# Kernel optimization log

Hardware: AMD Instinct MI355X
Metric: run time of the kernel (lower is better)

Reference implementation:

```python
import jax, jax.numpy as jnp
import numpy as np

NUM_HEADS = 8

def setup_inputs() -> dict:
    key = jax.random.key(0)
    k1, k2, k3, k4 = jax.random.split(key, 4)
    B, N, S, C = 16, 256, 4096, 512
    return {
        "query": jax.random.normal(k1, (B, N, C), dtype=jnp.float32),
        "key": jax.random.normal(k2, (B, S, C), dtype=jnp.float32),
        "Wq": jax.random.normal(k3, (C, C), dtype=jnp.float32) * (C ** -0.5),
        "Wk": jax.random.normal(k4, (C, C), dtype=jnp.float32) * (C ** -0.5),
    }

def reference(query, key, Wq, Wk):
    B, N, C = query.shape
    S = key.shape[1]
    H = NUM_HEADS
    hd = C // H
    scale = hd ** -0.5
    # value = key (v_proj is Identity, value defaults to key)
    q = (query @ Wq).reshape(B, N, H, hd)   # b n h c
    k = (key @ Wk).reshape(B, S, H, hd)     # b s h c
    raw_attn = jnp.einsum('bnhc,bshc->bhns', q, k) * scale  # [B,H,N,S]
    # softmax over the QUERY axis (dim=-2), non-standard
    attn = jax.nn.softmax(raw_attn, axis=-2)
    # clamp-normalize over token axis; divisor is detached in the original
    div = jnp.clip(jnp.sum(attn, axis=-1, keepdims=True), 1.0, None)
    attn = attn / jax.lax.stop_gradient(div)
    # attn_drop has p=0.0 -> identity
    v = key.reshape(B, S, H, hd)
    out = jnp.einsum('bhns,bshc->bnhc', attn, v).reshape(B, N, C)
    # out_style = attn @ key_heads; since value == key this equals out
    out_style = out
    return out, out_style
```

## Files before the change

### kernel.cpp

```cpp
#include <hip/hip_runtime.h>
#include <hip/hip_bf16.h>


typedef __attribute__((ext_vector_type(8))) short bf16x8;
typedef __attribute__((ext_vector_type(4))) float f32x4;
typedef unsigned int u32;

__device__ __forceinline__ unsigned short f2bf(float f) {
  union { __hip_bfloat16 h; unsigned short u; } cv;
  cv.h = __float2bfloat16(f);
  return cv.u;
}

__device__ __forceinline__ u32 pkbf(float a, float b) {
  union { __hip_bfloat162 h; u32 u; } cv;
  cv.h = __float22bfloat162_rn(float2{a, b});
  return cv.u;
}

__device__ __forceinline__ void async_copy16(const void* gptr, void* lptr) {
  __builtin_amdgcn_global_load_lds((const __attribute__((address_space(1))) u32*)gptr,
                                   (__attribute__((address_space(3))) u32*)lptr,
                                   16, 0, 0);
}

__global__ __launch_bounds__(256) void prep_w(const float* __restrict__ Wq,
                                              const float* __restrict__ Wk,
                                              unsigned short* __restrict__ WtQ,
                                              unsigned short* __restrict__ WtK) {
  __shared__ float tile[64][65];
  const int blk = blockIdx.x;
  const float* W = (blk & 1) ? Wk : Wq;
  unsigned short* Wt = (blk & 1) ? WtK : WtQ;
  const int tb = blk >> 1;
  const int k0 = (tb >> 3) * 64, n0 = (tb & 7) * 64;
  const int t = threadIdx.x;
  const int row = t >> 4, col4 = (t & 15) * 4;
#pragma unroll
  for (int i = 0; i < 4; ++i) {
    int r = i * 16 + row;
    float4 v = *reinterpret_cast<const float4*>(&W[(size_t)(k0 + r) * 512 + n0 + col4]);
    tile[r][col4 + 0] = v.x; tile[r][col4 + 1] = v.y;
    tile[r][col4 + 2] = v.z; tile[r][col4 + 3] = v.w;
  }
  __syncthreads();
#pragma unroll
  for (int i = 0; i < 4; ++i) {
    int r = i * 16 + row;
    short4 s;
    s.x = (short)f2bf(tile[col4 + 0][r]);
    s.y = (short)f2bf(tile[col4 + 1][r]);
    s.z = (short)f2bf(tile[col4 + 2][r]);
    s.w = (short)f2bf(tile[col4 + 3][r]);
    *reinterpret_cast<short4*>(&Wt[(size_t)(n0 + r) * 512 + k0 + col4]) = s;
  }
}

__global__ __launch_bounds__(256, 3) void gemm_xw(const float* __restrict__ X,
                                                  const unsigned short* __restrict__ Wt,
                                                  __hip_bfloat16* __restrict__ Y) {
  __shared__ float As[128 * 64];
  __shared__ unsigned short Bs[128 * 64];
  const int t = threadIdx.x;
  const int wave = t >> 6, lane = t & 63, l15 = lane & 15, quad = lane >> 4;
  const int n0 = blockIdx.x * 128, m0 = blockIdx.y * 128;
  const int wm = (wave >> 1) * 64, wn = (wave & 1) * 64;

  const int a_rl = lane >> 4;
  const int b_rl = lane >> 3;
  const int b_cs = (lane & 7) ^ b_rl;

  f32x4 acc[4][4];
#pragma unroll
  for (int i = 0; i < 4; ++i)
#pragma unroll
    for (int j = 0; j < 4; ++j) { f32x4 z = {0.f, 0.f, 0.f, 0.f}; acc[i][j] = z; }

  for (int k0 = 0; k0 < 512; k0 += 64) {
    __syncthreads();
    {
      const float* aBase = X + (size_t)m0 * 512 + k0;
#pragma unroll
      for (int o = 0; o < 8; ++o) {
        int rg = wave * 8 + o;
        int r = rg * 4 + a_rl;
        int cs = (lane & 15) ^ (r & 7);
        async_copy16(aBase + (size_t)r * 512 + cs * 4, &As[rg * 256]);
      }
      const unsigned short* bBase = Wt + (size_t)n0 * 512 + k0;
#pragma unroll
      for (int o = 0; o < 4; ++o) {
        int rg = wave * 4 + o;
        int r = rg * 8 + b_rl;
        async_copy16(bBase + (size_t)r * 512 + b_cs * 8, &Bs[rg * 512]);
      }
    }
    __syncthreads();

#pragma unroll
    for (int x = 0; x < 2; ++x) {
      bf16x8 a[4], bfr[4];
#pragma unroll
      for (int i = 0; i < 4; ++i) {
        int ra = wm + 16 * i + l15;
        int c0 = x * 8 + quad * 2;
        float4 f0 = *reinterpret_cast<const float4*>(&As[(ra * 16 + (c0 ^ (ra & 7))) * 4]);
        float4 f1 = *reinterpret_cast<const float4*>(&As[(ra * 16 + ((c0 + 1) ^ (ra & 7))) * 4]);
        union { bf16x8 v; unsigned short s[8]; } u;
        u.s[0] = f2bf(f0.x); u.s[1] = f2bf(f0.y); u.s[2] = f2bf(f0.z); u.s[3] = f2bf(f0.w);
        u.s[4] = f2bf(f1.x); u.s[5] = f2bf(f1.y); u.s[6] = f2bf(f1.z); u.s[7] = f2bf(f1.w);
        a[i] = u.v;
      }
#pragma unroll
      for (int j = 0; j < 4; ++j) {
        int rb = wn + 16 * j + l15;
        int cb = x * 4 + quad;
        bfr[j] = *reinterpret_cast<const bf16x8*>(&Bs[(rb * 8 + (cb ^ (rb & 7))) * 8]);
      }
#pragma unroll
      for (int i = 0; i < 4; ++i)
#pragma unroll
        for (int j = 0; j < 4; ++j)
          acc[i][j] = __builtin_amdgcn_mfma_f32_16x16x32_bf16(a[i], bfr[j], acc[i][j], 0, 0, 0);
    }
  }
#pragma unroll
  for (int i = 0; i < 4; ++i)
#pragma unroll
    for (int j = 0; j < 4; ++j)
#pragma unroll
      for (int r = 0; r < 4; ++r) {
        int m = m0 + wm + 16 * i + 4 * quad + r;
        int n = n0 + wn + 16 * j + l15;
        Y[(size_t)m * 512 + n] = __float2bfloat16(acc[i][j][r]);
      }
}

__global__ __launch_bounds__(512, 2) void attn_kernel(const __hip_bfloat16* __restrict__ qg,
                                                      const __hip_bfloat16* __restrict__ kg,
                                                      const float* __restrict__ keyg,
                                                      float* __restrict__ accg,
                                                      float* __restrict__ rsg) {
  __shared__ unsigned short qs[256 * 64];
  __shared__ unsigned short vs[64 * 128];
  __shared__ unsigned short pst[256 * 128];

  const int t = threadIdx.x;
  const int wave = t >> 6, lane = t & 63, l15 = lane & 15, quad = lane >> 4;
  const int blk = blockIdx.x, chunk = blk & 1, bh = blk >> 1, b = bh >> 3, h = bh & 7;
  const int l7 = l15 & 7;

  {
    const unsigned short* qbase = (const unsigned short*)qg + (size_t)(b * 256) * 512 + h * 64;
#pragma unroll
    for (int i = 0; i < 4; ++i) {
      int lin = i * 512 + t;
      int n = lin >> 3, cc = lin & 7, phys = cc ^ (n & 7);
      bf16x8 v = *reinterpret_cast<const bf16x8*>(qbase + (size_t)n * 512 + cc * 8);
      *reinterpret_cast<bf16x8*>(&qs[n * 64 + phys * 8]) = v;
    }
  }

  const unsigned short* kbase = (const unsigned short*)kg + (size_t)(b * 4096 + chunk * 2048) * 512 + h * 64;
  const float* vbase = keyg + (size_t)(b * 4096 + chunk * 2048) * 512 + h * 64;

  bf16x8 kc0 = *reinterpret_cast<const bf16x8*>(kbase + (size_t)(16 * wave + l15) * 512 + quad * 8);
  bf16x8 kc1 = *reinterpret_cast<const bf16x8*>(kbase + (size_t)(16 * wave + l15) * 512 + 32 + quad * 8);
  float vbuf[16];
#pragma unroll
  for (int half = 0; half < 2; ++half) {
    int sc = wave + 8 * half;
#pragma unroll
    for (int j = 0; j < 8; ++j)
      vbuf[half * 8 + j] = vbase[(size_t)(sc * 8 + j) * 512 + lane];
  }

  union { bf16x8 f; int w[4]; } ones_u;
  ones_u.w[0] = 0x3F803F80; ones_u.w[1] = 0x3F803F80;
  ones_u.w[2] = 0x3F803F80; ones_u.w[3] = 0x3F803F80;
  const bf16x8 ones = ones_u.f;

  f32x4 oacc[2][4], rsacc[2];
#pragma unroll
  for (int i = 0; i < 2; ++i) {
    f32x4 z = {0.f, 0.f, 0.f, 0.f};
    rsacc[i] = z;
#pragma unroll
    for (int j = 0; j < 4; ++j) oacc[i][j] = z;
  }

  __syncthreads();

  for (int it = 0; it < 16; ++it) {
    f32x4 L[16];
#pragma unroll
    for (int jt = 0; jt < 16; ++jt) { f32x4 z = {0.f, 0.f, 0.f, 0.f}; L[jt] = z; }
#pragma unroll
    for (int x = 0; x < 2; ++x) {
      bf16x8 kf = x ? kc1 : kc0;
#pragma unroll
      for (int jt = 0; jt < 16; ++jt) {
        bf16x8 bq = *reinterpret_cast<const bf16x8*>(
            &qs[(16 * jt + l15) * 64 + ((4 * x + quad) ^ l7) * 8]);
        L[jt] = __builtin_amdgcn_mfma_f32_16x16x32_bf16(kf, bq, L[jt], 0, 0, 0);
      }
    }

    const int nit = (it < 15) ? it + 1 : 15;
    kc0 = *reinterpret_cast<const bf16x8*>(kbase + (size_t)(nit * 128 + 16 * wave + l15) * 512 + quad * 8);
    kc1 = *reinterpret_cast<const bf16x8*>(kbase + (size_t)(nit * 128 + 16 * wave + l15) * 512 + 32 + quad * 8);

    float cs0 = 0.f, cs1 = 0.f, cs2 = 0.f, cs3 = 0.f;
#pragma unroll
    for (int jt = 0; jt < 16; ++jt) {
      float e0 = __expf(L[jt][0] * 0.125f);
      float e1 = __expf(L[jt][1] * 0.125f);
      float e2 = __expf(L[jt][2] * 0.125f);
      float e3 = __expf(L[jt][3] * 0.125f);
      L[jt][0] = e0; L[jt][1] = e1; L[jt][2] = e2; L[jt][3] = e3;
      cs0 += e0; cs1 += e1; cs2 += e2; cs3 += e3;
    }
#pragma unroll
    for (int m = 1; m <= 8; m <<= 1) {
      cs0 += __shfl_xor(cs0, m);
      cs1 += __shfl_xor(cs1, m);
      cs2 += __shfl_xor(cs2, m);
      cs3 += __shfl_xor(cs3, m);
    }
    const float ri0 = 1.0f / cs0, ri1 = 1.0f / cs1, ri2 = 1.0f / cs2, ri3 = 1.0f / cs3;

    __syncthreads();

#pragma unroll
    for (int half = 0; half < 2; ++half) {
      int sc = wave + 8 * half;
      uint4 w;
      w.x = pkbf(vbuf[half * 8 + 0], vbuf[half * 8 + 1]);
      w.y = pkbf(vbuf[half * 8 + 2], vbuf[half * 8 + 3]);
      w.z = pkbf(vbuf[half * 8 + 4], vbuf[half * 8 + 5]);
      w.w = pkbf(vbuf[half * 8 + 6], vbuf[half * 8 + 7]);
      *reinterpret_cast<uint4*>(&vs[lane * 128 + (sc ^ (lane & 7)) * 8]) = w;
    }

    {
      const int scw = 2 * wave + (quad >> 1);
      const int half8 = (quad & 1) * 4;
#pragma unroll
      for (int jt = 0; jt < 16; ++jt) {
        uint2 w;
        w.x = pkbf(L[jt][0] * ri0, L[jt][1] * ri1);
        w.y = pkbf(L[jt][2] * ri2, L[jt][3] * ri3);
        int row = 16 * jt + l15;
        *reinterpret_cast<uint2*>(&pst[row * 128 + ((scw ^ l7) * 8) + half8]) = w;
      }
    }

    __syncthreads();

#pragma unroll
    for (int half = 0; half < 2; ++half) {
      int sc = wave + 8 * half;
#pragma unroll
      for (int j = 0; j < 8; ++j)
        vbuf[half * 8 + j] = vbase[(size_t)(nit * 128 + sc * 8 + j) * 512 + lane];
    }

#pragma unroll
    for (int kc = 0; kc < 4; ++kc) {
      bf16x8 bv[4];
#pragma unroll
      for (int jc = 0; jc < 4; ++jc)
        bv[jc] = *reinterpret_cast<const bf16x8*>(
            &vs[(16 * jc + l15) * 128 + ((4 * kc + quad) ^ l7) * 8]);
#pragma unroll
      for (int jtl = 0; jtl < 2; ++jtl) {
        int rowp = 16 * (2 * wave + jtl) + l15;
        bf16x8 ap = *reinterpret_cast<const bf16x8*>(
            &pst[rowp * 128 + ((4 * kc + quad) ^ l7) * 8]);
#pragma unroll
        for (int jc = 0; jc < 4; ++jc)
          oacc[jtl][jc] = __builtin_amdgcn_mfma_f32_16x16x32_bf16(ap, bv[jc], oacc[jtl][jc], 0, 0, 0);
        rsacc[jtl] = __builtin_amdgcn_mfma_f32_16x16x32_bf16(ap, ones, rsacc[jtl], 0, 0, 0);
      }
    }
  }

  float* rsp = rsg + chunk * 32768 + bh * 256;
  if (l15 == 0) {
#pragma unroll
    for (int jtl = 0; jtl < 2; ++jtl)
#pragma unroll
      for (int r = 0; r < 4; ++r)
        rsp[16 * (2 * wave + jtl) + 4 * quad + r] = rsacc[jtl][r];
  }
  float* ap_ = accg + (size_t)chunk * 2097152 + (size_t)bh * 16384;
#pragma unroll
  for (int jtl = 0; jtl < 2; ++jtl)
#pragma unroll
    for (int jc = 0; jc < 4; ++jc)
#pragma unroll
      for (int r = 0; r < 4; ++r)
        ap_[(16 * (2 * wave + jtl) + 4 * quad + r) * 64 + 16 * jc + l15] = oacc[jtl][jc][r];
}

__global__ __launch_bounds__(256) void finalize(const float* __restrict__ acc,
                                                const float* __restrict__ rs,
                                                float* __restrict__ out) {
  int idx = blockIdx.x * 256 + threadIdx.x;
  int c = idx & 63, n = (idx >> 6) & 255, bh = idx >> 14;
  float v = acc[idx] + acc[idx + 2097152];
  float r = rs[bh * 256 + n] + rs[32768 + bh * 256 + n];
  float o = v / fmaxf(r, 1.0f);
  int b = bh >> 3, h = bh & 7;
  size_t oi = ((size_t)(b * 256 + n)) * 512 + h * 64 + c;
  out[oi] = o;
  out[oi + 2097152] = o;
}

extern "C" void kernel_launch(void* const* d_in, const int* in_sizes, int n_in,
                              void* d_out, int out_size, void* d_ws, size_t ws_size,
                              hipStream_t stream) {
  const float* query = (const float*)d_in[0];
  const float* key   = (const float*)d_in[1];
  const float* Wq    = (const float*)d_in[2];
  const float* Wk    = (const float*)d_in[3];
  float* out = (float*)d_out;
  char* ws = (char*)d_ws;

  unsigned short* WtQ = (unsigned short*)(ws);
  unsigned short* WtK = (unsigned short*)(ws + 524288);
  __hip_bfloat16* qbf = (__hip_bfloat16*)(ws + 1048576);
  __hip_bfloat16* kbf = (__hip_bfloat16*)(ws + 5242880);
  float* accw = (float*)(ws + 72351744);
  float* rsw  = (float*)(ws + 89128960);

  prep_w<<<128, 256, 0, stream>>>(Wq, Wk, WtQ, WtK);
  gemm_xw<<<dim3(4, 32), 256, 0, stream>>>(query, WtQ, qbf);
  gemm_xw<<<dim3(4, 512), 256, 0, stream>>>(key, WtK, kbf);
  attn_kernel<<<256, 512, 0, stream>>>(qbf, kbf, key, accw, rsw);
  finalize<<<8192, 256, 0, stream>>>(accw, rsw, out);
}
```

Baseline: 334.4 us.

## Convert A tile to bf16 at LDS store and remap workgroups for locality

The projection GEMM now loads the fp32 activation tile into registers, packs it to bf16 once, and stores bf16 into a swizzled LDS buffer. Previously the tile was copied as fp32 via async LDS loads and converted during every fragment read. This halves A's LDS footprint and removes the repeated conversions from the MFMA loop, which allows raising launch bounds to 4 blocks per CU. It also remaps block indices so neighbouring workgroups share rows, aiming for better cache reuse, at the cost of losing the async copy overlap for A.

```diff
diff --git a/kernel.cpp b/kernel.cpp
--- a/kernel.cpp
+++ b/kernel.cpp
@@ -56,17 +56,20 @@
   }
 }
 
-__global__ __launch_bounds__(256, 3) void gemm_xw(const float* __restrict__ X,
+__global__ __launch_bounds__(256, 4) void gemm_xw(const float* __restrict__ X,
                                                   const unsigned short* __restrict__ Wt,
                                                   __hip_bfloat16* __restrict__ Y) {
-  __shared__ float As[128 * 64];
+  __shared__ unsigned short As[128 * 64];
   __shared__ unsigned short Bs[128 * 64];
   const int t = threadIdx.x;
   const int wave = t >> 6, lane = t & 63, l15 = lane & 15, quad = lane >> 4;
-  const int n0 = blockIdx.x * 128, m0 = blockIdx.y * 128;
+
+  const int nwg = gridDim.x * gridDim.y;
+  const int d = blockIdx.y * gridDim.x + blockIdx.x;
+  const int tile = (d & 7) * (nwg >> 3) + (d >> 3);
+  const int n0 = (tile & 3) * 128, m0 = (tile >> 2) * 128;
+
   const int wm = (wave >> 1) * 64, wn = (wave & 1) * 64;
-
-  const int a_rl = lane >> 4;
   const int b_rl = lane >> 3;
   const int b_cs = (lane & 7) ^ b_rl;
 
@@ -78,22 +81,31 @@
 
   for (int k0 = 0; k0 < 512; k0 += 64) {
     __syncthreads();
+    float4 av[8];
     {
       const float* aBase = X + (size_t)m0 * 512 + k0;
 #pragma unroll
-      for (int o = 0; o < 8; ++o) {
-        int rg = wave * 8 + o;
-        int r = rg * 4 + a_rl;
-        int cs = (lane & 15) ^ (r & 7);
-        async_copy16(aBase + (size_t)r * 512 + cs * 4, &As[rg * 256]);
-      }
+      for (int i = 0; i < 8; ++i) {
+        int c = i * 256 + t;
+        av[i] = *reinterpret_cast<const float4*>(&aBase[(size_t)(c >> 4) * 512 + (c & 15) * 4]);
+      }
+    }
+    {
       const unsigned short* bBase = Wt + (size_t)n0 * 512 + k0;
 #pragma unroll
       for (int o = 0; o < 4; ++o) {
         int rg = wave * 4 + o;
-        int r = rg * 8 + b_rl;
-        async_copy16(bBase + (size_t)r * 512 + b_cs * 8, &Bs[rg * 512]);
-      }
+        async_copy16(bBase + (size_t)(rg * 8 + b_rl) * 512 + b_cs * 8, &Bs[rg * 512]);
+      }
+    }
+#pragma unroll
+    for (int i = 0; i < 8; ++i) {
+      int c = i * 256 + t;
+      int r = c >> 4, q4 = c & 15, cc = q4 >> 1, half = q4 & 1;
+      uint2 w2;
+      w2.x = pkbf(av[i].x, av[i].y);
+      w2.y = pkbf(av[i].z, av[i].w);
+      *reinterpret_cast<uint2*>(&As[r * 64 + ((cc ^ (r & 7)) << 3) + half * 4]) = w2;
     }
     __syncthreads();
 
@@ -103,19 +115,12 @@
 #pragma unroll
       for (int i = 0; i < 4; ++i) {
         int ra = wm + 16 * i + l15;
-        int c0 = x * 8 + quad * 2;
-        float4 f0 = *reinterpret_cast<const float4*>(&As[(ra * 16 + (c0 ^ (ra & 7))) * 4]);
-        float4 f1 = *reinterpret_cast<const float4*>(&As[(ra * 16 + ((c0 + 1) ^ (ra & 7))) * 4]);
-        union { bf16x8 v; unsigned short s[8]; } u;
-        u.s[0] = f2bf(f0.x); u.s[1] = f2bf(f0.y); u.s[2] = f2bf(f0.z); u.s[3] = f2bf(f0.w);
-        u.s[4] = f2bf(f1.x); u.s[5] = f2bf(f1.y); u.s[6] = f2bf(f1.z); u.s[7] = f2bf(f1.w);
-        a[i] = u.v;
+        a[i] = *reinterpret_cast<const bf16x8*>(&As[ra * 64 + (((x * 4 + quad) ^ (ra & 7)) << 3)]);
       }
 #pragma unroll
       for (int j = 0; j < 4; ++j) {
         int rb = wn + 16 * j + l15;
-        int cb = x * 4 + quad;
-        bfr[j] = *reinterpret_cast<const bf16x8*>(&Bs[(rb * 8 + (cb ^ (rb & 7))) * 8]);
+        bfr[j] = *reinterpret_cast<const bf16x8*>(&Bs[rb * 64 + (((x * 4 + quad) ^ (rb & 7)) << 3)]);
       }
 #pragma unroll
       for (int i = 0; i < 4; ++i)
```

Measured after the change: 387.0 us. 1.16x slower.
